# Kernel optimization log

Measured on AMD Instinct MI355X. Metric: run time of the kernel, lower is better.

Reference implementation:

```python
import jax, jax.numpy as jnp
import numpy as np


def setup_inputs() -> dict:
    key = jax.random.key(0)
    ks = jax.random.split(key, 7)
    B, S, D, R = 4, 4096, 1024, 16
    scale = 1.0 / np.sqrt(D)
    return {
        "x": jax.random.normal(ks[0], (B, S, D), dtype=jnp.float32),
        "W_qkv": jax.random.normal(ks[1], (3 * D, D), dtype=jnp.float32) * scale,
        "b_qkv": jax.random.normal(ks[2], (3 * D,), dtype=jnp.float32) * 0.02,
        "W_a_q": jax.random.normal(ks[3], (R, D), dtype=jnp.float32) * scale,
        "W_b_q": jnp.zeros((D, R), dtype=jnp.float32) + jax.random.normal(ks[4], (D, R), dtype=jnp.float32) * 0.02,
        "W_a_v": jax.random.normal(ks[5], (R, D), dtype=jnp.float32) * scale,
        "W_b_v": jax.random.normal(ks[6], (D, R), dtype=jnp.float32) * 0.02,
    }


def reference(x, W_qkv, b_qkv, W_a_q, W_b_q, W_a_v, W_b_v):
    D = W_a_q.shape[1]
    # base qkv projection: [B, S, 3D]
    qkv = jnp.einsum("bsd,ed->bse", x, W_qkv) + b_qkv
    # LoRA branches: x -> [B,S,r] -> [B,S,D]
    q_ba = jnp.einsum("bsr,dr->bsd", jnp.einsum("bsd,rd->bsr", x, W_a_q), W_b_q)
    v_ba = jnp.einsum("bsr,dr->bsd", jnp.einsum("bsd,rd->bsr", x, W_a_v), W_b_v)
    # add into q slice ([:D]) and v slice ([-D:])
    qkv = qkv.at[:, :, :D].add(q_ba)
    qkv = qkv.at[:, :, -D:].add(v_ba)
    return qkv
```

## Files before the change

### kernel.cpp

```cpp
#include <hip/hip_runtime.h>
#include <hip/hip_bf16.h>

typedef __bf16 bf16x4 __attribute__((ext_vector_type(4)));
typedef __bf16 bf16x8 __attribute__((ext_vector_type(8)));
typedef float floatx4 __attribute__((ext_vector_type(4)));

#define GLD16(gp, lp) __builtin_amdgcn_global_load_lds(                      \
    (const __attribute__((address_space(1))) void*)(gp),                     \
    (__attribute__((address_space(3))) void*)(lp), 16, 0, 0)

constexpr int Mdim = 16384;
constexpr int Ndim = 3072;
constexpr int Kdim = 1024;

static __device__ __forceinline__ bf16x8 cvt8(floatx4 lo, floatx4 hi) {
    bf16x8 r;
#pragma unroll
    for (int e = 0; e < 4; ++e) { r[e] = (__bf16)lo[e]; r[e + 4] = (__bf16)hi[e]; }
    return r;
}


__global__ __launch_bounds__(256) void build_weff(
    const float* __restrict__ Wqkv,
    const float* __restrict__ Waq,
    const float* __restrict__ Wbq,
    const float* __restrict__ Wav,
    const float* __restrict__ Wbv,
    __hip_bfloat16* __restrict__ Weff)
{
    const int idx = (blockIdx.x * 256 + threadIdx.x) * 4;
    const int e = idx >> 10;
    const int d = idx & 1023;
    floatx4 v = *(const floatx4*)(Wqkv + idx);
    if (e < 1024) {
#pragma unroll
        for (int r = 0; r < 16; ++r) {
            const float wb = Wbq[e * 16 + r];
            floatx4 wa = *(const floatx4*)(Waq + r * 1024 + d);
#pragma unroll
            for (int q = 0; q < 4; ++q) v[q] += wb * wa[q];
        }
    } else if (e >= 2048) {
        const int e2 = e - 2048;
#pragma unroll
        for (int r = 0; r < 16; ++r) {
            const float wb = Wbv[e2 * 16 + r];
            floatx4 wa = *(const floatx4*)(Wav + r * 1024 + d);
#pragma unroll
            for (int q = 0; q < 4; ++q) v[q] += wb * wa[q];
        }
    }
    bf16x4 o;
#pragma unroll
    for (int q = 0; q < 4; ++q) o[q] = (__bf16)v[q];
    *(bf16x4*)(Weff + idx) = o;
}

__global__ __launch_bounds__(256) void cvt_x(
    const float* __restrict__ x, __hip_bfloat16* __restrict__ xb)
{
    const size_t idx = ((size_t)blockIdx.x * 256 + threadIdx.x) * 8;
    bf16x8 r = cvt8(*(const floatx4*)(x + idx), *(const floatx4*)(x + idx + 4));
    *(bf16x8*)(xb + idx) = r;
}

__global__ __launch_bounds__(512, 2) void gemm_bf16_v6(
    const __hip_bfloat16* __restrict__ A,
    const __hip_bfloat16* __restrict__ Bw,
    const float* __restrict__ bias,
    float* __restrict__ C)
{
    constexpr int NT = Kdim / 64;
    __shared__ __align__(16) char smem[131072];

    const int t    = threadIdx.x;
    const int wid  = t >> 6;
    const int lane = t & 63;
    const int wm   = wid >> 2;
    const int wn   = wid & 3;

    constexpr int NWG = (Mdim / 256) * (Ndim / 256);
    const int bid = (blockIdx.x & 7) * (NWG >> 3) + (blockIdx.x >> 3);
    const int bx  = bid % (Ndim / 256);
    const int by  = bid / (Ndim / 256);
    const int m0  = by * 256;
    const int n0  = bx * 256;

    const int srow0 = t >> 3;
    const int scb   = ((t & 7) * 16) ^ ((srow0 & 7) << 4);
    const __hip_bfloat16* Ag = A  + (size_t)(m0 + srow0) * Kdim + (scb >> 1);
    const __hip_bfloat16* Bg = Bw + (size_t)(n0 + srow0) * Kdim + (scb >> 1);

#define STG(mat, h, kt_, b_) do {                                              \
    const __hip_bfloat16* _g = ((mat) ? Bg : Ag)                               \
        + (size_t)((h) * 128) * Kdim + (kt_) * 64;                             \
    char* _l = smem + (b_) * 65536 + (mat) * 32768 + (h) * 16384 + t * 16;     \
    GLD16(_g,                     _l);                                         \
    GLD16(_g + (size_t)64 * Kdim, _l + 8192);                                  \
} while (0)

    const int fm  = lane & 15;
    const int fk2 = (lane >> 4) * 16;
    const int fx  = (fm & 7) << 4;
    const int cb0 = fk2 ^ fx;
    const int cb1 = (64 + fk2) ^ fx;

    floatx4 acc[8][4];
#pragma unroll
    for (int i = 0; i < 8; ++i)
#pragma unroll
        for (int j = 0; j < 4; ++j)
            acc[i][j] = (floatx4){0.f, 0.f, 0.f, 0.f};

#define MFMA_Q(mq, nq, BQ)                                                     \
    __builtin_amdgcn_s_setprio(1);                                             \
    _Pragma("unroll")                                                          \
    for (int i = 0; i < 4; ++i)                                                \
        _Pragma("unroll")                                                      \
        for (int j = 0; j < 2; ++j) {                                          \
            acc[(mq) * 4 + i][(nq) * 2 + j] =                                  \
                __builtin_amdgcn_mfma_f32_16x16x32_bf16(                       \
                    aq[i][0], BQ[j][0], acc[(mq) * 4 + i][(nq) * 2 + j], 0,0,0);\
            acc[(mq) * 4 + i][(nq) * 2 + j] =                                  \
                __builtin_amdgcn_mfma_f32_16x16x32_bf16(                       \
                    aq[i][1], BQ[j][1], acc[(mq) * 4 + i][(nq) * 2 + j], 0,0,0);\
        }                                                                      \
    __builtin_amdgcn_s_setprio(0);

    STG(0, 0, 0, 0); STG(0, 1, 0, 0); STG(1, 0, 0, 0); STG(1, 1, 0, 0);
    STG(1, 0, 1, 1); STG(0, 0, 1, 1);

    bf16x8 aq[4][2], bq0[2][2], bq1[2][2];

    for (int kt = 0; kt < NT; ++kt) {
        const int b = kt & 1;
        const char* Ab = smem + b * 65536;
        const char* Bb = Ab + 32768;

        if (kt + 1 < NT) {
            STG(0, 1, kt + 1, b ^ 1);
            asm volatile("s_waitcnt vmcnt(6)" ::: "memory");
        } else {
            asm volatile("s_waitcnt vmcnt(0)" ::: "memory");
        }
        __builtin_amdgcn_s_barrier();
        __builtin_amdgcn_sched_barrier(0x8);
#pragma unroll
        for (int i = 0; i < 4; ++i) {
            const char* ar = Ab + (wm * 128 + i * 16 + fm) * 128;
            aq[i][0] = *(const bf16x8*)(ar + cb0);
            aq[i][1] = *(const bf16x8*)(ar + cb1);
        }
#pragma unroll
        for (int j = 0; j < 2; ++j) {
            const char* br = Bb + (wn * 64 + j * 16 + fm) * 128;
            bq0[j][0] = *(const bf16x8*)(br + cb0);
            bq0[j][1] = *(const bf16x8*)(br + cb1);
        }
        MFMA_Q(0, 0, bq0)

#pragma unroll
        for (int j = 0; j < 2; ++j) {
            const char* br = Bb + (wn * 64 + 32 + j * 16 + fm) * 128;
            bq1[j][0] = *(const bf16x8*)(br + cb0);
            bq1[j][1] = *(const bf16x8*)(br + cb1);
        }
        if (kt + 1 < NT) STG(1, 1, kt + 1, b ^ 1);
        MFMA_Q(0, 1, bq1)
        __builtin_amdgcn_s_barrier();
        __builtin_amdgcn_sched_barrier(0x108);

#pragma unroll
        for (int i = 0; i < 4; ++i) {
            const char* ar = Ab + (wm * 128 + 64 + i * 16 + fm) * 128;
            aq[i][0] = *(const bf16x8*)(ar + cb0);
            aq[i][1] = *(const bf16x8*)(ar + cb1);
        }
        if (kt + 2 < NT) STG(1, 0, kt + 2, b);
        MFMA_Q(1, 0, bq0)
        __builtin_amdgcn_s_barrier();
        __builtin_amdgcn_sched_barrier(0x108);

        if (kt + 2 < NT) STG(0, 0, kt + 2, b);
        MFMA_Q(1, 1, bq1)
    }

    const int cn = lane & 15;
    const int cm = (lane >> 4) * 4;
    float bv[4];
#pragma unroll
    for (int j = 0; j < 4; ++j)
        bv[j] = bias[n0 + wn * 64 + j * 16 + cn];

#pragma unroll
    for (int mi = 0; mi < 8; ++mi) {
        const int m = m0 + wm * 128 + mi * 16 + cm;
#pragma unroll
        for (int ni = 0; ni < 4; ++ni) {
            const int n = n0 + wn * 64 + ni * 16 + cn;
            const size_t base = (size_t)m * Ndim + n;
#pragma unroll
            for (int r = 0; r < 4; ++r)
                C[base + (size_t)r * Ndim] = acc[mi][ni][r] + bv[ni];
        }
    }
#undef STG
#undef MFMA_Q
}


__global__ __launch_bounds__(256, 2) void gemm_bias_f32(
    const float* __restrict__ A, const float* __restrict__ Bw,
    const float* __restrict__ bias, float* __restrict__ C)
{
    constexpr int TK = 32;
    __shared__ __hip_bfloat16 As[128 * TK];
    __shared__ __hip_bfloat16 Bs[128 * TK];

    const int t    = threadIdx.x;
    const int wave = t >> 6;
    const int lane = t & 63;
    const int bx   = blockIdx.x % (Ndim / 128);
    const int by   = blockIdx.x / (Ndim / 128);
    const int m0   = by * 128;
    const int n0   = bx * 128;
    const int wm   = wave >> 1;
    const int wn   = wave & 1;
    const int srow = wave * 16 + (lane >> 2);
    const int scol = (lane & 3) * 8;

    const float* Ag0 = A  + (size_t)(m0 + srow) * Kdim + scol;
    const float* Ag1 = Ag0 + (size_t)64 * Kdim;
    const float* Bg0 = Bw + (size_t)(n0 + srow) * Kdim + scol;
    const float* Bg1 = Bg0 + (size_t)64 * Kdim;

    __hip_bfloat16* Al0 = &As[srow * TK + scol];
    __hip_bfloat16* Al1 = &As[(srow + 64) * TK + scol];
    __hip_bfloat16* Bl0 = &Bs[srow * TK + scol];
    __hip_bfloat16* Bl1 = &Bs[(srow + 64) * TK + scol];

    const int fm = lane & 15;
    const int fk = (lane >> 4) * 8;

    floatx4 acc[4][4];
#pragma unroll
    for (int i = 0; i < 4; ++i)
#pragma unroll
        for (int j = 0; j < 4; ++j)
            acc[i][j] = (floatx4){0.f, 0.f, 0.f, 0.f};

    for (int kt = 0; kt < Kdim; kt += TK) {
        bf16x8 a0 = cvt8(*(const floatx4*)(Ag0 + kt), *(const floatx4*)(Ag0 + kt + 4));
        bf16x8 a1 = cvt8(*(const floatx4*)(Ag1 + kt), *(const floatx4*)(Ag1 + kt + 4));
        bf16x8 b0 = cvt8(*(const floatx4*)(Bg0 + kt), *(const floatx4*)(Bg0 + kt + 4));
        bf16x8 b1 = cvt8(*(const floatx4*)(Bg1 + kt), *(const floatx4*)(Bg1 + kt + 4));
        __syncthreads();
        *(bf16x8*)Al0 = a0;
        *(bf16x8*)Al1 = a1;
        *(bf16x8*)Bl0 = b0;
        *(bf16x8*)Bl1 = b1;
        __syncthreads();

        bf16x8 af[4], bfr[4];
#pragma unroll
        for (int i = 0; i < 4; ++i) {
            af[i]  = *(const bf16x8*)&As[(wm * 64 + i * 16 + fm) * TK + fk];
            bfr[i] = *(const bf16x8*)&Bs[(wn * 64 + i * 16 + fm) * TK + fk];
        }
#pragma unroll
        for (int i = 0; i < 4; ++i)
#pragma unroll
            for (int j = 0; j < 4; ++j)
                acc[i][j] = __builtin_amdgcn_mfma_f32_16x16x32_bf16(af[i], bfr[j], acc[i][j], 0, 0, 0);
    }

    const int cn = lane & 15;
    const int cm = (lane >> 4) * 4;
    float bv[4];
#pragma unroll
    for (int j = 0; j < 4; ++j)
        bv[j] = bias[n0 + wn * 64 + j * 16 + cn];
#pragma unroll
    for (int i = 0; i < 4; ++i) {
        const int m = m0 + wm * 64 + i * 16 + cm;
#pragma unroll
        for (int j = 0; j < 4; ++j) {
            const int n = n0 + wn * 64 + j * 16 + cn;
            const size_t base = (size_t)m * Ndim + n;
#pragma unroll
            for (int r = 0; r < 4; ++r)
                C[base + (size_t)r * Ndim] = acc[i][j][r] + bv[j];
        }
    }
}

__global__ __launch_bounds__(256) void lora_rmw(
    const float* __restrict__ x,
    const float* __restrict__ Waq, const float* __restrict__ Wbq,
    const float* __restrict__ Wav, const float* __restrict__ Wbv,
    float* __restrict__ out)
{
    __shared__ float Pq[64][16];
    __shared__ float Pv[64][16];
    const int t  = threadIdx.x;
    const int m0 = blockIdx.x * 64;
    {
        const int row = t >> 2;
        const int r0  = (t & 3) * 4;
        float accq[4] = {0.f, 0.f, 0.f, 0.f};
        float accv[4] = {0.f, 0.f, 0.f, 0.f};
        const float* xr = x + (size_t)(m0 + row) * Kdim;
        for (int d = 0; d < Kdim; d += 4) {
            floatx4 xv = *(const floatx4*)(xr + d);
#pragma unroll
            for (int rr = 0; rr < 4; ++rr) {
                floatx4 wq = *(const floatx4*)(Waq + (size_t)(r0 + rr) * Kdim + d);
                floatx4 wv = *(const floatx4*)(Wav + (size_t)(r0 + rr) * Kdim + d);
#pragma unroll
                for (int e = 0; e < 4; ++e) {
                    accq[rr] += xv[e] * wq[e];
                    accv[rr] += xv[e] * wv[e];
                }
            }
        }
#pragma unroll
        for (int rr = 0; rr < 4; ++rr) {
            Pq[row][r0 + rr] = accq[rr];
            Pv[row][r0 + rr] = accv[rr];
        }
    }
    __syncthreads();
    const int col  = t * 8;
    const bool isq = col < 1024;
    const int nn0  = isq ? col : col - 1024;
    const int n    = isq ? col : col + 1024;
    const float* Wb = isq ? Wbq : Wbv;
    for (int row = 0; row < 64; ++row) {
        const float* P = isq ? Pq[row] : Pv[row];
        const size_t off = (size_t)(m0 + row) * Ndim + n;
        floatx4 o0 = *(const floatx4*)(out + off);
        floatx4 o1 = *(const floatx4*)(out + off + 4);
#pragma unroll
        for (int i = 0; i < 8; ++i) {
            floatx4 w0 = *(const floatx4*)(Wb + (size_t)(nn0 + i) * 16);
            floatx4 w1 = *(const floatx4*)(Wb + (size_t)(nn0 + i) * 16 + 4);
            floatx4 w2 = *(const floatx4*)(Wb + (size_t)(nn0 + i) * 16 + 8);
            floatx4 w3 = *(const floatx4*)(Wb + (size_t)(nn0 + i) * 16 + 12);
            float s = 0.f;
#pragma unroll
            for (int r = 0; r < 4; ++r)
                s += P[r] * w0[r] + P[r + 4] * w1[r] + P[r + 8] * w2[r] + P[r + 12] * w3[r];
            if (i < 4) o0[i] += s; else o1[i - 4] += s;
        }
        *(floatx4*)(out + off)     = o0;
        *(floatx4*)(out + off + 4) = o1;
    }
}

extern "C" void kernel_launch(void* const* d_in, const int* in_sizes, int n_in,
                              void* d_out, int out_size, void* d_ws, size_t ws_size,
                              hipStream_t stream)
{
    (void)in_sizes; (void)n_in; (void)out_size;
    const float* x    = (const float*)d_in[0];
    const float* Wqkv = (const float*)d_in[1];
    const float* bqkv = (const float*)d_in[2];
    const float* Waq  = (const float*)d_in[3];
    const float* Wbq  = (const float*)d_in[4];
    const float* Wav  = (const float*)d_in[5];
    const float* Wbv  = (const float*)d_in[6];
    float* out = (float*)d_out;

    const size_t WEFF_BYTES = (size_t)Ndim * Kdim * sizeof(__hip_bfloat16);
    const size_t XB_BYTES   = (size_t)Mdim * Kdim * sizeof(__hip_bfloat16);

    if (ws_size >= WEFF_BYTES + XB_BYTES) {
        __hip_bfloat16* Weff = (__hip_bfloat16*)d_ws;
        __hip_bfloat16* xb   = (__hip_bfloat16*)((char*)d_ws + WEFF_BYTES);
        build_weff<<<(Ndim * Kdim / 4) / 256, 256, 0, stream>>>(Wqkv, Waq, Wbq, Wav, Wbv, Weff);
        cvt_x<<<(int)(((size_t)Mdim * Kdim / 8) / 256), 256, 0, stream>>>(x, xb);
        gemm_bf16_v6<<<(Mdim / 256) * (Ndim / 256), 512, 0, stream>>>(xb, Weff, bqkv, out);
    } else {
        gemm_bias_f32<<<(Mdim / 128) * (Ndim / 128), 256, 0, stream>>>(x, Wqkv, bqkv, out);
        lora_rmw<<<Mdim / 64, 256, 0, stream>>>(x, Waq, Wbq, Wav, Wbv, out);
    }
}
```

Before: 360.3 us.

## Make GEMM persistent over three N-tiles per workgroup and fuse prep kernels

The two preprocessing kernels (folding LoRA into bf16 effective weights, converting x to bf16) are merged into one launch split by block index. The GEMM now launches 256 workgroups, each computing three consecutive 256-wide N tiles for one M block. The double-buffered K pipeline runs straight across tile boundaries, so the prefetch for the next tile overlaps the epilogue store of the current one. This targets the tail effect of 768 workgroups on 256 CUs and per-tile pipeline fill/drain. The cost is longer per-block serial work and an A tile that gets reloaded for each N tile.

```diff
diff --git a/kernel.cpp b/kernel.cpp
--- a/kernel.cpp
+++ b/kernel.cpp
@@ -21,57 +21,59 @@
 }
 
 
-__global__ __launch_bounds__(256) void build_weff(
+__global__ __launch_bounds__(256) void prep(
+    const float* __restrict__ x,
     const float* __restrict__ Wqkv,
     const float* __restrict__ Waq,
     const float* __restrict__ Wbq,
     const float* __restrict__ Wav,
     const float* __restrict__ Wbv,
-    __hip_bfloat16* __restrict__ Weff)
+    __hip_bfloat16* __restrict__ Weff,
+    __hip_bfloat16* __restrict__ xb)
 {
-    const int idx = (blockIdx.x * 256 + threadIdx.x) * 4;
-    const int e = idx >> 10;
-    const int d = idx & 1023;
-    floatx4 v = *(const floatx4*)(Wqkv + idx);
-    if (e < 1024) {
-#pragma unroll
-        for (int r = 0; r < 16; ++r) {
-            const float wb = Wbq[e * 16 + r];
-            floatx4 wa = *(const floatx4*)(Waq + r * 1024 + d);
-#pragma unroll
-            for (int q = 0; q < 4; ++q) v[q] += wb * wa[q];
-        }
-    } else if (e >= 2048) {
-        const int e2 = e - 2048;
-#pragma unroll
-        for (int r = 0; r < 16; ++r) {
-            const float wb = Wbv[e2 * 16 + r];
-            floatx4 wa = *(const floatx4*)(Wav + r * 1024 + d);
-#pragma unroll
-            for (int q = 0; q < 4; ++q) v[q] += wb * wa[q];
-        }
-    }
-    bf16x4 o;
-#pragma unroll
-    for (int q = 0; q < 4; ++q) o[q] = (__bf16)v[q];
-    *(bf16x4*)(Weff + idx) = o;
-}
-
-__global__ __launch_bounds__(256) void cvt_x(
-    const float* __restrict__ x, __hip_bfloat16* __restrict__ xb)
-{
-    const size_t idx = ((size_t)blockIdx.x * 256 + threadIdx.x) * 8;
-    bf16x8 r = cvt8(*(const floatx4*)(x + idx), *(const floatx4*)(x + idx + 4));
-    *(bf16x8*)(xb + idx) = r;
-}
-
-__global__ __launch_bounds__(512, 2) void gemm_bf16_v6(
+    if (blockIdx.x < 3072) {
+        const int idx = (blockIdx.x * 256 + threadIdx.x) * 4;
+        const int e = idx >> 10;
+        const int d = idx & 1023;
+        floatx4 v = *(const floatx4*)(Wqkv + idx);
+        if (e < 1024) {
+#pragma unroll
+            for (int r = 0; r < 16; ++r) {
+                const float wb = Wbq[e * 16 + r];
+                floatx4 wa = *(const floatx4*)(Waq + r * 1024 + d);
+#pragma unroll
+                for (int q = 0; q < 4; ++q) v[q] += wb * wa[q];
+            }
+        } else if (e >= 2048) {
+            const int e2 = e - 2048;
+#pragma unroll
+            for (int r = 0; r < 16; ++r) {
+                const float wb = Wbv[e2 * 16 + r];
+                floatx4 wa = *(const floatx4*)(Wav + r * 1024 + d);
+#pragma unroll
+                for (int q = 0; q < 4; ++q) v[q] += wb * wa[q];
+            }
+        }
+        bf16x4 o;
+#pragma unroll
+        for (int q = 0; q < 4; ++q) o[q] = (__bf16)v[q];
+        *(bf16x4*)(Weff + idx) = o;
+    } else {
+        const size_t idx = ((size_t)(blockIdx.x - 3072) * 256 + threadIdx.x) * 8;
+        bf16x8 r = cvt8(*(const floatx4*)(x + idx), *(const floatx4*)(x + idx + 4));
+        *(bf16x8*)(xb + idx) = r;
+    }
+}
+
+__global__ __launch_bounds__(512, 2) void gemm_bf16_v7(
     const __hip_bfloat16* __restrict__ A,
     const __hip_bfloat16* __restrict__ Bw,
     const float* __restrict__ bias,
     float* __restrict__ C)
 {
-    constexpr int NT = Kdim / 64;
+    constexpr int NT  = Kdim / 64;
+    constexpr int TPB = 3;
+    constexpr int NVK = NT * TPB;
     __shared__ __align__(16) char smem[131072];
 
     const int t    = threadIdx.x;
@@ -80,21 +82,21 @@
     const int wm   = wid >> 2;
     const int wn   = wid & 3;
 
-    constexpr int NWG = (Mdim / 256) * (Ndim / 256);
-    const int bid = (blockIdx.x & 7) * (NWG >> 3) + (blockIdx.x >> 3);
-    const int bx  = bid % (Ndim / 256);
-    const int by  = bid / (Ndim / 256);
-    const int m0  = by * 256;
-    const int n0  = bx * 256;
+    const int bid  = (blockIdx.x & 7) * 32 + (blockIdx.x >> 3);
+    const int m0   = (bid >> 2) * 256;
+    const int n_b  = (bid & 3) * TPB * 256;
 
     const int srow0 = t >> 3;
     const int scb   = ((t & 7) * 16) ^ ((srow0 & 7) << 4);
-    const __hip_bfloat16* Ag = A  + (size_t)(m0 + srow0) * Kdim + (scb >> 1);
-    const __hip_bfloat16* Bg = Bw + (size_t)(n0 + srow0) * Kdim + (scb >> 1);
-
-#define STG(mat, h, kt_, b_) do {                                              \
-    const __hip_bfloat16* _g = ((mat) ? Bg : Ag)                               \
-        + (size_t)((h) * 128) * Kdim + (kt_) * 64;                             \
+    const __hip_bfloat16* Ag  = A  + (size_t)(m0 + srow0) * Kdim + (scb >> 1);
+    const __hip_bfloat16* Bg0 = Bw + (size_t)srow0 * Kdim + (scb >> 1);
+
+#define STG(mat, h, vk_, b_) do {                                              \
+    const int _vk = (vk_);                                                     \
+    const __hip_bfloat16* _g;                                                  \
+    if (mat) _g = Bg0 + (size_t)(n_b + (_vk >> 4) * 256 + (h) * 128) * Kdim    \
+                  + (_vk & 15) * 64;                                           \
+    else     _g = Ag + (size_t)((h) * 128) * Kdim + (_vk & 15) * 64;           \
     char* _l = smem + (b_) * 65536 + (mat) * 32768 + (h) * 16384 + t * 16;     \
     GLD16(_g,                     _l);                                         \
     GLD16(_g + (size_t)64 * Kdim, _l + 8192);                                  \
@@ -105,6 +107,8 @@
     const int fx  = (fm & 7) << 4;
     const int cb0 = fk2 ^ fx;
     const int cb1 = (64 + fk2) ^ fx;
+    const int cn  = lane & 15;
+    const int cm  = (lane >> 4) * 4;
 
     floatx4 acc[8][4];
 #pragma unroll
@@ -128,85 +132,105 @@
         }                                                                      \
     __builtin_amdgcn_s_setprio(0);
 
+#define STORE_TILE(N0_) do {                                                   \
+    _Pragma("unroll")                                                          \
+    for (int mi = 0; mi < 8; ++mi) {                                           \
+        const int m = m0 + wm * 128 + mi * 16 + cm;                            \
+        _Pragma("unroll")                                                      \
+        for (int ni = 0; ni < 4; ++ni) {                                       \
+            const int n = (N0_) + wn * 64 + ni * 16 + cn;                      \
+            const size_t base = (size_t)m * Ndim + n;                          \
+            _Pragma("unroll")                                                  \
+            for (int r = 0; r < 4; ++r)                                        \
+                C[base + (size_t)r * Ndim] = acc[mi][ni][r] + bv[ni];          \
+        }                                                                      \
+    }                                                                          \
+} while (0)
+
+    int n0 = n_b;
+    float bv[4];
+#pragma unroll
+    for (int j = 0; j < 4; ++j)
+        bv[j] = bias[n0 + wn * 64 + j * 16 + cn];
+
     STG(0, 0, 0, 0); STG(0, 1, 0, 0); STG(1, 0, 0, 0); STG(1, 1, 0, 0);
     STG(1, 0, 1, 1); STG(0, 0, 1, 1);
 
     bf16x8 aq[4][2], bq0[2][2], bq1[2][2];
 
-    for (int kt = 0; kt < NT; ++kt) {
-        const int b = kt & 1;
-        const char* Ab = smem + b * 65536;
-        const char* Bb = Ab + 32768;
-
-        if (kt + 1 < NT) {
-            STG(0, 1, kt + 1, b ^ 1);
-            asm volatile("s_waitcnt vmcnt(6)" ::: "memory");
-        } else {
-            asm volatile("s_waitcnt vmcnt(0)" ::: "memory");
-        }
-        __builtin_amdgcn_s_barrier();
-        __builtin_amdgcn_sched_barrier(0x8);
-#pragma unroll
-        for (int i = 0; i < 4; ++i) {
-            const char* ar = Ab + (wm * 128 + i * 16 + fm) * 128;
-            aq[i][0] = *(const bf16x8*)(ar + cb0);
-            aq[i][1] = *(const bf16x8*)(ar + cb1);
-        }
-#pragma unroll
-        for (int j = 0; j < 2; ++j) {
-            const char* br = Bb + (wn * 64 + j * 16 + fm) * 128;
-            bq0[j][0] = *(const bf16x8*)(br + cb0);
-            bq0[j][1] = *(const bf16x8*)(br + cb1);
-        }
-        MFMA_Q(0, 0, bq0)
-
-#pragma unroll
-        for (int j = 0; j < 2; ++j) {
-            const char* br = Bb + (wn * 64 + 32 + j * 16 + fm) * 128;
-            bq1[j][0] = *(const bf16x8*)(br + cb0);
-            bq1[j][1] = *(const bf16x8*)(br + cb1);
-        }
-        if (kt + 1 < NT) STG(1, 1, kt + 1, b ^ 1);
-        MFMA_Q(0, 1, bq1)
-        __builtin_amdgcn_s_barrier();
-        __builtin_amdgcn_sched_barrier(0x108);
-
-#pragma unroll
-        for (int i = 0; i < 4; ++i) {
-            const char* ar = Ab + (wm * 128 + 64 + i * 16 + fm) * 128;
-            aq[i][0] = *(const bf16x8*)(ar + cb0);
-            aq[i][1] = *(const bf16x8*)(ar + cb1);
-        }
-        if (kt + 2 < NT) STG(1, 0, kt + 2, b);
-        MFMA_Q(1, 0, bq0)
-        __builtin_amdgcn_s_barrier();
-        __builtin_amdgcn_sched_barrier(0x108);
-
-        if (kt + 2 < NT) STG(0, 0, kt + 2, b);
-        MFMA_Q(1, 1, bq1)
-    }
-
-    const int cn = lane & 15;
-    const int cm = (lane >> 4) * 4;
-    float bv[4];
-#pragma unroll
-    for (int j = 0; j < 4; ++j)
-        bv[j] = bias[n0 + wn * 64 + j * 16 + cn];
-
-#pragma unroll
-    for (int mi = 0; mi < 8; ++mi) {
-        const int m = m0 + wm * 128 + mi * 16 + cm;
-#pragma unroll
-        for (int ni = 0; ni < 4; ++ni) {
-            const int n = n0 + wn * 64 + ni * 16 + cn;
-            const size_t base = (size_t)m * Ndim + n;
-#pragma unroll
-            for (int r = 0; r < 4; ++r)
-                C[base + (size_t)r * Ndim] = acc[mi][ni][r] + bv[ni];
-        }
-    }
+#pragma unroll 1
+    for (int tile = 0; tile < TPB; ++tile) {
+        for (int kt = 0; kt < NT; ++kt) {
+            const int vkt = tile * NT + kt;
+            const int b   = vkt & 1;
+            const char* Ab = smem + b * 65536;
+            const char* Bb = Ab + 32768;
+
+            if (vkt + 1 < NVK) {
+                STG(0, 1, vkt + 1, b ^ 1);
+                asm volatile("s_waitcnt vmcnt(6)" ::: "memory");
+            } else {
+                asm volatile("s_waitcnt vmcnt(0)" ::: "memory");
+            }
+            __builtin_amdgcn_s_barrier();
+            __builtin_amdgcn_sched_barrier(0x8);
+#pragma unroll
+            for (int i = 0; i < 4; ++i) {
+                const char* ar = Ab + (wm * 128 + i * 16 + fm) * 128;
+                aq[i][0] = *(const bf16x8*)(ar + cb0);
+                aq[i][1] = *(const bf16x8*)(ar + cb1);
+            }
+#pragma unroll
+            for (int j = 0; j < 2; ++j) {
+                const char* br = Bb + (wn * 64 + j * 16 + fm) * 128;
+                bq0[j][0] = *(const bf16x8*)(br + cb0);
+                bq0[j][1] = *(const bf16x8*)(br + cb1);
+            }
+            MFMA_Q(0, 0, bq0)
+
+#pragma unroll
+            for (int j = 0; j < 2; ++j) {
+                const char* br = Bb + (wn * 64 + 32 + j * 16 + fm) * 128;
+                bq1[j][0] = *(const bf16x8*)(br + cb0);
+                bq1[j][1] = *(const bf16x8*)(br + cb1);
+            }
+            if (vkt + 1 < NVK) STG(1, 1, vkt + 1, b ^ 1);
+            MFMA_Q(0, 1, bq1)
+            __builtin_amdgcn_s_barrier();
+            __builtin_amdgcn_sched_barrier(0x108);
+
+#pragma unroll
+            for (int i = 0; i < 4; ++i) {
+                const char* ar = Ab + (wm * 128 + 64 + i * 16 + fm) * 128;
+                aq[i][0] = *(const bf16x8*)(ar + cb0);
+                aq[i][1] = *(const bf16x8*)(ar + cb1);
+            }
+            if (vkt + 2 < NVK) STG(1, 0, vkt + 2, b);
+            MFMA_Q(1, 0, bq0)
+            __builtin_amdgcn_s_barrier();
+            __builtin_amdgcn_sched_barrier(0x108);
+
+            if (vkt + 2 < NVK) STG(0, 0, vkt + 2, b);
+            MFMA_Q(1, 1, bq1)
+        }
+        if (tile + 1 < TPB) {
+            STORE_TILE(n0);
+#pragma unroll
+            for (int i = 0; i < 8; ++i)
+#pragma unroll
+                for (int j = 0; j < 4; ++j)
+                    acc[i][j] = (floatx4){0.f, 0.f, 0.f, 0.f};
+            n0 += 256;
+#pragma unroll
+            for (int j = 0; j < 4; ++j)
+                bv[j] = bias[n0 + wn * 64 + j * 16 + cn];
+        }
+    }
+
+    STORE_TILE(n0);
 #undef STG
 #undef MFMA_Q
+#undef STORE_TILE
 }
 
 
@@ -378,9 +402,8 @@
     if (ws_size >= WEFF_BYTES + XB_BYTES) {
         __hip_bfloat16* Weff = (__hip_bfloat16*)d_ws;
         __hip_bfloat16* xb   = (__hip_bfloat16*)((char*)d_ws + WEFF_BYTES);
-        build_weff<<<(Ndim * Kdim / 4) / 256, 256, 0, stream>>>(Wqkv, Waq, Wbq, Wav, Wbv, Weff);
-        cvt_x<<<(int)(((size_t)Mdim * Kdim / 8) / 256), 256, 0, stream>>>(x, xb);
-        gemm_bf16_v6<<<(Mdim / 256) * (Ndim / 256), 512, 0, stream>>>(xb, Weff, bqkv, out);
+        prep<<<3072 + 8192, 256, 0, stream>>>(x, Wqkv, Waq, Wbq, Wav, Wbv, Weff, xb);
+        gemm_bf16_v7<<<256, 512, 0, stream>>>(xb, Weff, bqkv, out);
     } else {
         gemm_bias_f32<<<(Mdim / 128) * (Ndim / 128), 256, 0, stream>>>(x, Wqkv, bqkv, out);
         lora_rmw<<<Mdim / 64, 256, 0, stream>>>(x, Waq, Wbq, Wav, Wbv, out);
```

Result: no change. 359.4 us (-0.2%).
